# Performance work log

Hardware: AMD Instinct MI355X
Metric: run time of the kernel (lower is better)

The kernel has to match this reference:

```python
import jax, jax.numpy as jnp
import numpy as np

K = 32        # neighbors kept
SCALE = 1     # dilation stride for dilated kNN


def setup_inputs() -> dict:
    key = jax.random.key(0)
    ks = jax.random.split(key, 8)
    s = 0.05  # weight init scale
    return {
        "x": jax.random.normal(ks[0], (16, 3, 4096), jnp.float32),
        "w1": jax.random.normal(ks[1], (64, 3), jnp.float32) * s,
        "b1": jnp.zeros((64,), jnp.float32),
        "w2": jax.random.normal(ks[2], (128, 64), jnp.float32) * s,
        "b2": jnp.zeros((128,), jnp.float32),
        "w3": jax.random.normal(ks[3], (1024, 128), jnp.float32) * s,
        "b3": jnp.zeros((1024,), jnp.float32),
        "fw1": jax.random.normal(ks[4], (512, 1024), jnp.float32) * s,
        "fb1": jnp.zeros((512,), jnp.float32),
        "fw2": jax.random.normal(ks[5], (256, 512), jnp.float32) * s,
        "fb2": jnp.zeros((256,), jnp.float32),
        "fw3": jax.random.normal(ks[6], (9, 256), jnp.float32) * s,
        "fb3": jnp.zeros((9,), jnp.float32),
    }


def _knn_idx(x):
    # x: (B, C, N). Returns (B, N, K) indices of K nearest neighbors (dilated by SCALE).
    inner = jnp.einsum('bcn,bcm->bnm', x, x)            # (B, N, N)
    sq = jnp.sum(x * x, axis=1)                          # (B, N)
    neg_dist = 2.0 * inner - sq[:, :, None] - sq[:, None, :]  # = -||xi-xj||^2
    _, idx = jax.lax.top_k(neg_dist, K * SCALE)          # (B, N, K*SCALE)
    return idx[:, :, ::SCALE]                            # (B, N, K)


def reference(x, w1, b1, w2, b2, w3, b3, fw1, fb1, fw2, fb2, fw3, fb3):
    B, C, N = x.shape
    idx = _knn_idx(x)                                    # (B, N, K)
    xt = jnp.swapaxes(x, 1, 2)                           # (B, N, C)
    # gather neighbors: nbrs[b,n,k,c] = xt[b, idx[b,n,k], c]
    nbrs = jax.vmap(lambda xb, ib: xb[ib])(xt, idx)      # (B, N, K, C)
    x0 = nbrs - xt[:, :, None, :]                        # edge features x_j - x_i

    # STN (T-Net): shared MLP over edges, global max pool, FC head -> 3x3 transform
    h = jax.nn.relu(jnp.einsum('bnkc,oc->bnko', x0, w1) + b1)
    h = jax.nn.relu(jnp.einsum('bnkc,oc->bnko', h, w2) + b2)
    h = jax.nn.relu(jnp.einsum('bnkc,oc->bnko', h, w3) + b3)
    g = jnp.max(h, axis=(1, 2))                          # (B, 1024)
    f = jax.nn.relu(g @ fw1.T + fb1)
    f = jax.nn.relu(f @ fw2.T + fb2)
    t = (f @ fw3.T + fb3).reshape(B, 3, 3) + jnp.eye(3, dtype=x.dtype)

    out = jnp.einsum('bnc,bcd->bnd', xt, t)              # bmm(x^T, t)
    return jnp.swapaxes(out, 1, 2)                       # (B, 3, N)
```

## Files before the change

kernel.cpp:

```cpp
#include <hip/hip_runtime.h>
#include <hip/hip_fp8.h>

typedef __bf16 bf16_t;
typedef __bf16 bf16x8 __attribute__((ext_vector_type(8)));
typedef float floatx16 __attribute__((ext_vector_type(16)));
typedef int intx8 __attribute__((ext_vector_type(8)));
typedef unsigned long long u64;

#define B_ 16
#define N_ 4096
#define K_ 32


__device__ __forceinline__ unsigned enc_f(float f) {
    unsigned u = __float_as_uint(f);
    return (u & 0x80000000u) ? ~u : (u | 0x80000000u);
}
__device__ __forceinline__ float dec_f(unsigned e) {
    return __uint_as_float((e & 0x80000000u) ? (e & 0x7fffffffu) : ~e);
}

__device__ __forceinline__ float max3f(float a, float b, float c) {
    float d;
    asm("v_max3_f32 %0, %1, %2, %3" : "=v"(d) : "v"(a), "v"(b), "v"(c));
    return d;
}

__device__ __forceinline__ void ce(unsigned& a, unsigned& b) {
    const unsigned mn = a < b ? a : b;
    const unsigned mx = a < b ? b : a;
    a = mn; b = mx;
}

__device__ __forceinline__ void sort8(unsigned* k) {
    ce(k[0], k[1]); ce(k[2], k[3]); ce(k[4], k[5]); ce(k[6], k[7]);
    ce(k[0], k[2]); ce(k[1], k[3]); ce(k[4], k[6]); ce(k[5], k[7]);
    ce(k[1], k[2]); ce(k[5], k[6]);
    ce(k[0], k[4]); ce(k[1], k[5]); ce(k[2], k[6]); ce(k[3], k[7]);
    ce(k[2], k[4]); ce(k[3], k[5]);
    ce(k[1], k[2]); ce(k[3], k[4]); ce(k[5], k[6]);
}
__device__ __forceinline__ void merge_top8(unsigned* r, const unsigned* k) {
    unsigned s[8];
    #pragma unroll
    for (int u = 0; u < 8; u++)
        s[u] = r[u] < k[7 - u] ? r[u] : k[7 - u];
    ce(s[0], s[4]); ce(s[1], s[5]); ce(s[2], s[6]); ce(s[3], s[7]);
    ce(s[0], s[2]); ce(s[1], s[3]); ce(s[4], s[6]); ce(s[5], s[7]);
    ce(s[0], s[1]); ce(s[2], s[3]); ce(s[4], s[5]); ce(s[6], s[7]);
    #pragma unroll
    for (int u = 0; u < 8; u++) r[u] = s[u];
}

__global__ __launch_bounds__(512) void prep_kernel(
    const float* __restrict__ w3, const float* __restrict__ w2,
    unsigned* __restrict__ g_enc, unsigned char* __restrict__ w3f8,
    bf16_t* __restrict__ w2sw)
{
    const int g = blockIdx.x * 512 + threadIdx.x;
    if (g < 131072) {
        const int j  = g & 31;
        const int lI = (g >> 5) & 63;
        const int kq = (g >> 11) & 1;
        const int cb = g >> 12;
        const int mt2 = kq * 2 + (j >> 4), q = j & 15;
        const int lmI = lI & 31, hiI = lI >> 5;
        const int ch = mt2 * 32 + (q & 3) + 8 * (q >> 2) + 4 * hiI;
        __hip_fp8_e4m3 t(16.0f * w3[(cb * 32 + lmI) * 128 + ch]);
        w3f8[g] = t.__x;
    } else if (g < 139264) {
        const int o = g - 131072;
        const int f = o >> 9, r = o & 511, lI = r >> 3, jj = r & 7;
        const int ks = f & 3, nb = f >> 2, lmI = lI & 31, hiI = lI >> 5;
        const int ic = ks * 16 + 4 * hiI + 8 * (jj >> 2) + (jj & 3);
        w2sw[o] = (bf16_t)w2[(nb * 32 + lmI) * 64 + ic];
    } else if (g < 155648) {
        g_enc[g - 139264] = 0u;
    }
}

__device__ __forceinline__ void chunk_epilogue(
    const floatx16& a0, const floatx16& a1, int cb, unsigned* gl, int lm)
{
    float c0 = fmaxf(a0[0], a1[0]);
    float c1 = fmaxf(a0[1], a1[1]);
    float c2 = fmaxf(a0[2], a1[2]);
    float c3 = fmaxf(a0[3], a1[3]);
    #pragma unroll
    for (int o = 4; o < 16; o += 4) {
        c0 = max3f(a0[o + 0], a1[o + 0], c0);
        c1 = max3f(a0[o + 1], a1[o + 1], c1);
        c2 = max3f(a0[o + 2], a1[o + 2], c2);
        c3 = max3f(a0[o + 3], a1[o + 3], c3);
    }
    const float m = max3f(c0, c1, fmaxf(c2, c3));
    atomicMax(&gl[cb * 32 + lm], enc_f(m));
}

__global__ __launch_bounds__(512, 2) void fused_kernel(
    const float* __restrict__ x,
    const float* __restrict__ w1, const float* __restrict__ b1,
    const float* __restrict__ b2,
    const bf16_t* __restrict__ w2sw, const unsigned char* __restrict__ w3f8,
    unsigned* __restrict__ g_enc)
{
    __shared__ __align__(16) char smem[65792];
    float4* cand = (float4*)smem;
    unsigned* lists = (unsigned*)smem;
    unsigned* m1 = ((unsigned*)smem) + 8192;
    unsigned short* idxl = (unsigned short*)smem;
    unsigned* gl = (unsigned*)(smem + 2048);
    float4* w1l = (float4*)(smem + 6144);
    float* b2s = (float*)(smem + 7168);

    const int tid = threadIdx.x;
    const int bid = blockIdx.x;
    const int b = bid >> 7;
    const int pbase = (bid & 127) * 32;
    const float* xb = x + b * 3 * N_;

    for (int j = tid; j < N_; j += 512) {
        float cx = xb[j], cy = xb[N_ + j], cz = xb[2 * N_ + j];
        cand[j + (j >> 8)] = make_float4(-2.f * cx, -2.f * cy, -2.f * cz,
                                         fmaf(cx, cx, fmaf(cy, cy, cz * cz)));
    }
    __syncthreads();

    {
        const int q = tid >> 4;
        const int n = pbase + q;
        const int t = tid & 15;
        const float xi0 = xb[n], xi1 = xb[N_ + n], xi2 = xb[2 * N_ + n];
        const float xisq1 = fmaf(xi0, xi0, fmaf(xi1, xi1, xi2 * xi2)) + 1.0f;

        unsigned r[8];
        #pragma unroll
        for (int s = 0; s < 8; s++) r[s] = 0x7F7FFFFFu;

        const int j0 = t * 256;
        const int pb = t * 257;
        #pragma unroll 1
        for (int jb = 0; jb < 256; jb += 8) {
            unsigned k[8];
            #pragma unroll
            for (int u = 0; u < 8; u++) {
                const float4 c = cand[pb + jb + u];
                const float d = fmaf(c.z, xi2, fmaf(c.y, xi1, fmaf(c.x, xi0, c.w)));
                k[u] = (__float_as_uint(d + xisq1) & 0xFFFFF000u)
                     | (unsigned)(j0 + jb + u);
            }
            sort8(k);
            merge_top8(r, k);
        }
        __syncthreads();

        #pragma unroll
        for (int k = 0; k < 8; k++) lists[tid * 9 + k] = r[k];
    }
    __syncthreads();

    if (tid < 128) {
        const int q1 = tid >> 2, gi = tid & 3;
        const int base = (q1 * 16 + gi * 4) * 9;
        unsigned h0 = lists[base], h1 = lists[base + 9];
        unsigned h2 = lists[base + 18], h3 = lists[base + 27];
        int p0 = 0, p1 = 0, p2 = 0, p3 = 0;
        unsigned* outp = m1 + (q1 * 4 + gi) * 33;
        #pragma unroll 1
        for (int k = 0; k < 32; k++) {
            const unsigned m01 = h0 < h1 ? h0 : h1;
            const unsigned m23 = h2 < h3 ? h2 : h3;
            const unsigned v = m01 < m23 ? m01 : m23;
            outp[k] = v;
            if (m01 < m23) {
                if (h1 < h0) { p1++; h1 = p1 < 8 ? lists[base + 9 + p1] : 0xFFFFFFFFu; }
                else         { p0++; h0 = p0 < 8 ? lists[base + p0]     : 0xFFFFFFFFu; }
            } else {
                if (h3 < h2) { p3++; h3 = p3 < 8 ? lists[base + 27 + p3] : 0xFFFFFFFFu; }
                else         { p2++; h2 = p2 < 8 ? lists[base + 18 + p2] : 0xFFFFFFFFu; }
            }
        }
    }
    __syncthreads();

    if (tid < 32) {
        const unsigned* l0 = m1 + (tid * 4 + 0) * 33;
        const unsigned* l1 = m1 + (tid * 4 + 1) * 33;
        const unsigned* l2 = m1 + (tid * 4 + 2) * 33;
        const unsigned* l3 = m1 + (tid * 4 + 3) * 33;
        unsigned h0 = l0[0], h1 = l1[0], h2 = l2[0], h3 = l3[0];
        int p0 = 0, p1 = 0, p2 = 0, p3 = 0;
        unsigned short* op = idxl + tid * 32;
        #pragma unroll 1
        for (int k = 0; k < K_; k++) {
            const unsigned m01 = h0 < h1 ? h0 : h1;
            const unsigned m23 = h2 < h3 ? h2 : h3;
            const unsigned v = m01 < m23 ? m01 : m23;
            op[k] = (unsigned short)(v & 0xFFFu);
            if (m01 < m23) {
                if (h1 < h0) { p1++; h1 = p1 < 32 ? l1[p1] : 0xFFFFFFFFu; }
                else         { p0++; h0 = p0 < 32 ? l0[p0] : 0xFFFFFFFFu; }
            } else {
                if (h3 < h2) { p3++; h3 = p3 < 32 ? l3[p3] : 0xFFFFFFFFu; }
                else         { p2++; h2 = p2 < 32 ? l2[p2] : 0xFFFFFFFFu; }
            }
        }
    } else if (tid >= 64 && tid < 128) {
        const int i = tid - 64;
        w1l[i] = make_float4(w1[i * 3], w1[i * 3 + 1], w1[i * 3 + 2], b1[i]);
    } else if (tid >= 128 && tid < 256) {
        b2s[tid - 128] = 256.0f * b2[tid - 128];
    } else if (tid >= 256) {
        for (int ii = tid - 256; ii < 1024; ii += 256) gl[ii] = 0u;
    }
    __syncthreads();

    const int wv = tid >> 6;
    const int l  = tid & 63;
    const int lm = l & 31;
    const int hi = l >> 5;
    const floatx16 zf = (floatx16)0.f;
    const unsigned char* w3p = w3f8 + l * 32;

#define PREFETCH_W3(dst, c) do {                                              \
        dst[0] = *(const intx8*)(w3p + (c) * 4096);                           \
        dst[1] = *(const intx8*)(w3p + (c) * 4096 + 2048);                    \
    } while (0)

#define COMPUTE_W3(d0_, d1_, buf) do {                                        \
        __builtin_amdgcn_s_setprio(1);                                        \
        d0_ = __builtin_amdgcn_mfma_scale_f32_32x32x64_f8f6f4(                \
            a3v[0][0], buf[0], zf, 0, 0, 0, 0x7F7F7F7F, 0, 0x7F7F7F7F);       \
        d1_ = __builtin_amdgcn_mfma_scale_f32_32x32x64_f8f6f4(                \
            a3v[1][0], buf[0], zf, 0, 0, 0, 0x7F7F7F7F, 0, 0x7F7F7F7F);       \
        d0_ = __builtin_amdgcn_mfma_scale_f32_32x32x64_f8f6f4(                \
            a3v[0][1], buf[1], d0_, 0, 0, 0, 0x7F7F7F7F, 0, 0x7F7F7F7F);      \
        d1_ = __builtin_amdgcn_mfma_scale_f32_32x32x64_f8f6f4(                \
            a3v[1][1], buf[1], d1_, 0, 0, 0, 0x7F7F7F7F, 0, 0x7F7F7F7F);      \
        __builtin_amdgcn_s_setprio(0); } while (0)

    #pragma unroll 1
    for (int it = 0; it < 2; it++) {
        intx8 bwA[2], bwB[2];
        PREFETCH_W3(bwA, 0);

        float d0[2], d1[2], d2[2];
        #pragma unroll
        for (int nt2 = 0; nt2 < 2; nt2++) {
            const int lp = wv * 4 + it * 2 + nt2;
            const int pp = pbase + lp;
            const int j  = idxl[lp * 32 + lm];
            d0[nt2] = xb[j]          - xb[pp];
            d1[nt2] = xb[N_ + j]     - xb[N_ + pp];
            d2[nt2] = xb[2 * N_ + j] - xb[2 * N_ + pp];
        }

        bf16x8 a1f[2];
        #pragma unroll
        for (int tt = 0; tt < 2; tt++) {
            const float4 w = w1l[tt * 32 + lm];
            bf16x8 v = (bf16x8)(bf16_t)0.f;
            if (hi == 0) {
                v[0] = (bf16_t)w.x; v[1] = (bf16_t)w.y;
                v[2] = (bf16_t)w.z; v[3] = (bf16_t)w.w;
            }
            a1f[tt] = v;
        }

        bf16x8 b1h[2][4];
        #pragma unroll
        for (int nt2 = 0; nt2 < 2; nt2++) {
            bf16x8 bf = (bf16x8)(bf16_t)0.f;
            if (hi == 0) {
                bf[0] = (bf16_t)d0[nt2]; bf[1] = (bf16_t)d1[nt2];
                bf[2] = (bf16_t)d2[nt2]; bf[3] = (bf16_t)1.0f;
            }
            floatx16 hacc[2];
            hacc[0] = __builtin_amdgcn_mfma_f32_32x32x16_bf16(a1f[0], bf, zf, 0, 0, 0);
            hacc[1] = __builtin_amdgcn_mfma_f32_32x32x16_bf16(a1f[1], bf, zf, 0, 0, 0);
            #pragma unroll
            for (int ks = 0; ks < 4; ks++)
                #pragma unroll
                for (int jj = 0; jj < 8; jj++)
                    b1h[nt2][ks][jj] = (bf16_t)fmaxf(
                        hacc[ks >> 1][(jj & 3) + 4 * (jj >> 2) + 8 * (ks & 1)], 0.f);
        }

        intx8 a3v[2][2];
        #pragma unroll
        for (int mt2 = 0; mt2 < 4; mt2++) {
            floatx16 acc0 = (floatx16)0.f, acc1 = (floatx16)0.f;
            #pragma unroll
            for (int ks = 0; ks < 4; ks++) {
                const bf16x8 aw = *(const bf16x8*)&w2sw[((mt2 * 4 + ks) * 64 + l) * 8];
                acc0 = __builtin_amdgcn_mfma_f32_32x32x16_bf16(aw, b1h[0][ks], acc0, 0, 0, 0);
                acc1 = __builtin_amdgcn_mfma_f32_32x32x16_bf16(aw, b1h[1][ks], acc1, 0, 0, 0);
            }
            const int kq = mt2 >> 1, c0 = (mt2 & 1) * 4;
            #pragma unroll
            for (int i2 = 0; i2 < 4; i2++) {
                const float4 bb = *(const float4*)&b2s[mt2 * 32 + i2 * 8 + hi * 4];
                {
                    const float v0 = fmaxf(fmaf(acc0[4 * i2 + 0], 256.f, bb.x), 0.f);
                    const float v1 = fmaxf(fmaf(acc0[4 * i2 + 1], 256.f, bb.y), 0.f);
                    const float v2 = fmaxf(fmaf(acc0[4 * i2 + 2], 256.f, bb.z), 0.f);
                    const float v3 = fmaxf(fmaf(acc0[4 * i2 + 3], 256.f, bb.w), 0.f);
                    int w = __builtin_amdgcn_cvt_pk_fp8_f32(v0, v1, 0, false);
                    w = __builtin_amdgcn_cvt_pk_fp8_f32(v2, v3, w, true);
                    a3v[0][kq][c0 + i2] = w;
                }
                {
                    const float v0 = fmaxf(fmaf(acc1[4 * i2 + 0], 256.f, bb.x), 0.f);
                    const float v1 = fmaxf(fmaf(acc1[4 * i2 + 1], 256.f, bb.y), 0.f);
                    const float v2 = fmaxf(fmaf(acc1[4 * i2 + 2], 256.f, bb.z), 0.f);
                    const float v3 = fmaxf(fmaf(acc1[4 * i2 + 3], 256.f, bb.w), 0.f);
                    int w = __builtin_amdgcn_cvt_pk_fp8_f32(v0, v1, 0, false);
                    w = __builtin_amdgcn_cvt_pk_fp8_f32(v2, v3, w, true);
                    a3v[1][kq][c0 + i2] = w;
                }
            }
        }

        floatx16 pA0, pA1, pB0, pB1;
        PREFETCH_W3(bwB, 1);
        COMPUTE_W3(pA0, pA1, bwA);
        #pragma unroll 1
        for (int cc = 0; cc < 15; cc++) {
            PREFETCH_W3(bwA, 2 * cc + 2);
            COMPUTE_W3(pB0, pB1, bwB);
            chunk_epilogue(pA0, pA1, 2 * cc, gl, lm);
            PREFETCH_W3(bwB, 2 * cc + 3);
            COMPUTE_W3(pA0, pA1, bwA);
            chunk_epilogue(pB0, pB1, 2 * cc + 1, gl, lm);
        }
        COMPUTE_W3(pB0, pB1, bwB);
        chunk_epilogue(pA0, pA1, 30, gl, lm);
        chunk_epilogue(pB0, pB1, 31, gl, lm);
    }

#undef PREFETCH_W3
#undef COMPUTE_W3

    __syncthreads();
    for (int i = tid; i < 1024; i += 512)
        atomicMax(&g_enc[b * 1024 + i], gl[i]);
}

__global__ __launch_bounds__(256) void head1_kernel(
    const unsigned* __restrict__ g_enc, const float* __restrict__ b3,
    const float* __restrict__ fw1, const float* __restrict__ fb1,
    float* __restrict__ f1buf)
{
    __shared__ __align__(16) float g[1024];
    __shared__ float red[256];
    const int t = threadIdx.x;
    const int b = blockIdx.x >> 3;
    const int s = blockIdx.x & 7;

    for (int i = t; i < 1024; i += 256)
        g[i] = fmaxf(fmaf(dec_f(g_enc[b * 1024 + i]), 2.44140625e-4f, b3[i]), 0.f);
    __syncthreads();

    const int o = s * 64 + (t & 63);
    const int quarter = t >> 6;
    const float4* wr = (const float4*)(fw1 + (size_t)o * 1024) + quarter * 64;
    const float4* gv = (const float4*)g + quarter * 64;
    float acc = 0.f;
    #pragma unroll 4
    for (int i = 0; i < 64; i++) {
        float4 a = wr[i], c = gv[i];
        acc = fmaf(a.x, c.x, acc); acc = fmaf(a.y, c.y, acc);
        acc = fmaf(a.z, c.z, acc); acc = fmaf(a.w, c.w, acc);
    }
    red[t] = acc;
    __syncthreads();
    if (t < 64) {
        const float v = red[t] + red[t + 64] + red[t + 128] + red[t + 192];
        f1buf[b * 512 + s * 64 + t] = fmaxf(v + fb1[s * 64 + t], 0.f);
    }
}

__global__ __launch_bounds__(256) void head2_kernel(
    const float* __restrict__ f1buf,
    const float* __restrict__ fw2, const float* __restrict__ fb2,
    const float* __restrict__ fw3, const float* __restrict__ fb3,
    float* __restrict__ tmat)
{
    __shared__ __align__(16) float f1[512];
    __shared__ __align__(16) float f2[256];
    const int t = threadIdx.x, b = blockIdx.x;

    if (t < 128) ((float4*)f1)[t] = ((const float4*)(f1buf + b * 512))[t];
    __syncthreads();
    {
        const int o = t;
        const float4* wr = (const float4*)(fw2 + (size_t)o * 512);
        const float4* fv = (const float4*)f1;
        float acc = fb2[o];
        for (int i = 0; i < 128; i++) {
            float4 a = wr[i], c = fv[i];
            acc = fmaf(a.x, c.x, acc); acc = fmaf(a.y, c.y, acc);
            acc = fmaf(a.z, c.z, acc); acc = fmaf(a.w, c.w, acc);
        }
        f2[o] = fmaxf(acc, 0.f);
    }
    __syncthreads();
    if (t < 9) {
        const float4* wr = (const float4*)(fw3 + (size_t)t * 256);
        const float4* fv = (const float4*)f2;
        float acc = fb3[t];
        for (int i = 0; i < 64; i++) {
            float4 a = wr[i], c = fv[i];
            acc = fmaf(a.x, c.x, acc); acc = fmaf(a.y, c.y, acc);
            acc = fmaf(a.z, c.z, acc); acc = fmaf(a.w, c.w, acc);
        }
        if (t == 0 || t == 4 || t == 8) acc += 1.f;
        tmat[b * 9 + t] = acc;
    }
}

__global__ __launch_bounds__(256) void out_kernel(
    const float* __restrict__ x, const float* __restrict__ tmat,
    float* __restrict__ out)
{
    const int gid = blockIdx.x * 256 + threadIdx.x;
    const int b = gid >> 12, n = gid & 4095;
    const float* T = tmat + b * 9;
    const float x0 = x[b * 12288 + n];
    const float x1 = x[b * 12288 + 4096 + n];
    const float x2 = x[b * 12288 + 8192 + n];
    #pragma unroll
    for (int d = 0; d < 3; d++)
        out[b * 12288 + d * 4096 + n] =
            fmaf(x2, T[6 + d], fmaf(x1, T[3 + d], x0 * T[d]));
}

extern "C" void kernel_launch(void* const* d_in, const int* in_sizes, int n_in,
                              void* d_out, int out_size, void* d_ws, size_t ws_size,
                              hipStream_t stream) {
    const float* x   = (const float*)d_in[0];
    const float* w1  = (const float*)d_in[1];
    const float* b1  = (const float*)d_in[2];
    const float* w2  = (const float*)d_in[3];
    const float* b2  = (const float*)d_in[4];
    const float* w3  = (const float*)d_in[5];
    const float* b3  = (const float*)d_in[6];
    const float* fw1 = (const float*)d_in[7];
    const float* fb1 = (const float*)d_in[8];
    const float* fw2 = (const float*)d_in[9];
    const float* fb2 = (const float*)d_in[10];
    const float* fw3 = (const float*)d_in[11];
    const float* fb3 = (const float*)d_in[12];
    float* out = (float*)d_out;

    char* ws = (char*)d_ws;
    unsigned* g_enc = (unsigned*)(ws + 4194304);
    unsigned char* w3f8 = (unsigned char*)(ws + 4259840);
    bf16_t* w2sw = (bf16_t*)(ws + 4390912);
    float* tmat  = (float*)(ws + 4407296);
    float* f1buf = (float*)(ws + 4407872);

    prep_kernel<<<304, 512, 0, stream>>>(w3, w2, g_enc, w3f8, w2sw);
    fused_kernel<<<2048, 512, 0, stream>>>(x, w1, b1, b2, w2sw, w3f8, g_enc);
    head1_kernel<<<128, 256, 0, stream>>>(g_enc, b3, fw1, fb1, f1buf);
    head2_kernel<<<16, 256, 0, stream>>>(f1buf, fw2, fb2, fw3, fb3, tmat);
    out_kernel<<<256, 256, 0, stream>>>(x, tmat, out);
}
```

Before: 547.8 us.

## Halve fused block to 256 threads with two-pass candidate staging in LDS

Shrinks the fused kNN+MLP block from 512 to 256 threads handling 16 points, with half the shared memory, so more blocks fit per CU. Candidates are staged into LDS in two 2048-point passes instead of all 4096 at once. The inner loop now sorts two 8-element groups and merges them before the running top-8. The costs are an extra pass of candidate loads and barriers per block, twice as many blocks, and more global atomics on the pooled max per output.

```diff
diff --git a/kernel.cpp b/kernel.cpp
--- a/kernel.cpp
+++ b/kernel.cpp
@@ -97,34 +97,27 @@
     atomicMax(&gl[cb * 32 + lm], enc_f(m));
 }
 
-__global__ __launch_bounds__(512, 2) void fused_kernel(
+__global__ __launch_bounds__(256, 3) void fused_kernel(
     const float* __restrict__ x,
     const float* __restrict__ w1, const float* __restrict__ b1,
     const float* __restrict__ b2,
     const bf16_t* __restrict__ w2sw, const unsigned char* __restrict__ w3f8,
     unsigned* __restrict__ g_enc)
 {
-    __shared__ __align__(16) char smem[65792];
+    __shared__ __align__(16) char smem[32896];
     float4* cand = (float4*)smem;
     unsigned* lists = (unsigned*)smem;
-    unsigned* m1 = ((unsigned*)smem) + 8192;
+    unsigned* m1 = (unsigned*)(smem + 9216);
     unsigned short* idxl = (unsigned short*)smem;
-    unsigned* gl = (unsigned*)(smem + 2048);
-    float4* w1l = (float4*)(smem + 6144);
-    float* b2s = (float*)(smem + 7168);
+    unsigned* gl = (unsigned*)(smem + 1024);
+    float4* w1l = (float4*)(smem + 5120);
+    float* b2s = (float*)(smem + 6144);
 
     const int tid = threadIdx.x;
     const int bid = blockIdx.x;
-    const int b = bid >> 7;
-    const int pbase = (bid & 127) * 32;
+    const int b = bid >> 8;
+    const int pbase = (bid & 255) * 16;
     const float* xb = x + b * 3 * N_;
-
-    for (int j = tid; j < N_; j += 512) {
-        float cx = xb[j], cy = xb[N_ + j], cz = xb[2 * N_ + j];
-        cand[j + (j >> 8)] = make_float4(-2.f * cx, -2.f * cy, -2.f * cz,
-                                         fmaf(cx, cx, fmaf(cy, cy, cz * cz)));
-    }
-    __syncthreads();
 
     {
         const int q = tid >> 4;
@@ -137,20 +130,42 @@
         #pragma unroll
         for (int s = 0; s < 8; s++) r[s] = 0x7F7FFFFFu;
 
-        const int j0 = t * 256;
-        const int pb = t * 257;
+        const int pb = t * 128 + (t >> 1);
+
         #pragma unroll 1
-        for (int jb = 0; jb < 256; jb += 8) {
-            unsigned k[8];
-            #pragma unroll
-            for (int u = 0; u < 8; u++) {
-                const float4 c = cand[pb + jb + u];
-                const float d = fmaf(c.z, xi2, fmaf(c.y, xi1, fmaf(c.x, xi0, c.w)));
-                k[u] = (__float_as_uint(d + xisq1) & 0xFFFFF000u)
-                     | (unsigned)(j0 + jb + u);
-            }
-            sort8(k);
-            merge_top8(r, k);
+        for (int pass = 0; pass < 2; pass++) {
+            __syncthreads();
+            for (int j = tid; j < 2048; j += 256) {
+                const int jg = pass * 2048 + j;
+                float cx = xb[jg], cy = xb[N_ + jg], cz = xb[2 * N_ + jg];
+                cand[j + (j >> 8)] = make_float4(-2.f * cx, -2.f * cy, -2.f * cz,
+                                                 fmaf(cx, cx, fmaf(cy, cy, cz * cz)));
+            }
+            __syncthreads();
+
+            const int j0 = pass * 2048 + t * 128;
+            #pragma unroll 1
+            for (int jb = 0; jb < 128; jb += 16) {
+                unsigned ka[8], kb[8];
+                #pragma unroll
+                for (int u = 0; u < 8; u++) {
+                    const float4 c = cand[pb + jb + u];
+                    const float d = fmaf(c.z, xi2, fmaf(c.y, xi1, fmaf(c.x, xi0, c.w)));
+                    ka[u] = (__float_as_uint(d + xisq1) & 0xFFFFF000u)
+                          | (unsigned)(j0 + jb + u);
+                }
+                #pragma unroll
+                for (int u = 0; u < 8; u++) {
+                    const float4 c = cand[pb + jb + 8 + u];
+                    const float d = fmaf(c.z, xi2, fmaf(c.y, xi1, fmaf(c.x, xi0, c.w)));
+                    kb[u] = (__float_as_uint(d + xisq1) & 0xFFFFF000u)
+                          | (unsigned)(j0 + jb + 8 + u);
+                }
+                sort8(ka);
+                sort8(kb);
+                merge_top8(ka, kb);
+                merge_top8(r, ka);
+            }
         }
         __syncthreads();
 
@@ -159,7 +174,7 @@
     }
     __syncthreads();
 
-    if (tid < 128) {
+    if (tid < 64) {
         const int q1 = tid >> 2, gi = tid & 3;
         const int base = (q1 * 16 + gi * 4) * 9;
         unsigned h0 = lists[base], h1 = lists[base + 9];
@@ -183,7 +198,7 @@
     }
     __syncthreads();
 
-    if (tid < 32) {
+    if (tid < 16) {
         const unsigned* l0 = m1 + (tid * 4 + 0) * 33;
         const unsigned* l1 = m1 + (tid * 4 + 1) * 33;
         const unsigned* l2 = m1 + (tid * 4 + 2) * 33;
@@ -208,10 +223,10 @@
     } else if (tid >= 64 && tid < 128) {
         const int i = tid - 64;
         w1l[i] = make_float4(w1[i * 3], w1[i * 3 + 1], w1[i * 3 + 2], b1[i]);
-    } else if (tid >= 128 && tid < 256) {
-        b2s[tid - 128] = 256.0f * b2[tid - 128];
-    } else if (tid >= 256) {
-        for (int ii = tid - 256; ii < 1024; ii += 256) gl[ii] = 0u;
+    } else if (tid >= 128) {
+        const int i = tid - 128;
+        b2s[i] = 256.0f * b2[i];
+        for (int ii = i; ii < 1024; ii += 128) gl[ii] = 0u;
     }
     __syncthreads();
 
@@ -342,7 +357,7 @@
 #undef COMPUTE_W3
 
     __syncthreads();
-    for (int i = tid; i < 1024; i += 512)
+    for (int i = tid; i < 1024; i += 256)
         atomicMax(&g_enc[b * 1024 + i], gl[i]);
 }
 
@@ -461,7 +476,7 @@
     float* f1buf = (float*)(ws + 4407872);
 
     prep_kernel<<<304, 512, 0, stream>>>(w3, w2, g_enc, w3f8, w2sw);
-    fused_kernel<<<2048, 512, 0, stream>>>(x, w1, b1, b2, w2sw, w3f8, g_enc);
+    fused_kernel<<<4096, 256, 0, stream>>>(x, w1, b1, b2, w2sw, w3f8, g_enc);
     head1_kernel<<<128, 256, 0, stream>>>(g_enc, b3, fw1, fb1, f1buf);
     head2_kernel<<<16, 256, 0, stream>>>(f1buf, fw2, fb2, fw3, fb3, tmat);
     out_kernel<<<256, 256, 0, stream>>>(x, tmat, out);
```

Result: no change. 555.1 us (+1.3%).
